# Optimization experiments

Hardware: AMD Instinct MI355X
Metric: run time of the kernel (lower is better)

## Reference

```python
import jax, jax.numpy as jnp
import numpy as np
from jax import lax

CONF_THRES = 0.25
IOU_THRES = 0.45
MAX_WH = 4096.0   # class offset, agnostic=False
MAX_DET = 300
NEG = jnp.float32(-1e30)


def setup_inputs() -> dict:
    key = jax.random.key(0)
    B, N, C = 16, 25200, 85  # 640x640 yolov5, nc=80
    k1, k2, k3, k4 = jax.random.split(key, 4)
    xy = jax.random.uniform(k1, (B, N, 2), jnp.float32, 0.0, 640.0)
    wh = jax.random.uniform(k2, (B, N, 2), jnp.float32, 4.0, 120.0)
    obj = jax.random.uniform(k3, (B, N, 1), jnp.float32)
    cls = jax.random.uniform(k4, (B, N, C - 5), jnp.float32)
    prediction = jnp.concatenate([xy, wh, obj, cls], axis=-1)
    return {"prediction": prediction}


def _xywh2xyxy(b):
    # b: [N,4] (cx,cy,w,h) -> (x1,y1,x2,y2)
    return jnp.concatenate([b[:, :2] - b[:, 2:4] * 0.5,
                            b[:, :2] + b[:, 2:4] * 0.5], axis=1)


def _iou_one_vs_all(box, boxes):
    # box: [4], boxes: [N,4], plain IoU as in torchvision.ops.nms
    x1 = jnp.maximum(box[0], boxes[:, 0])
    y1 = jnp.maximum(box[1], boxes[:, 1])
    x2 = jnp.minimum(box[2], boxes[:, 2])
    y2 = jnp.minimum(box[3], boxes[:, 3])
    inter = jnp.clip(x2 - x1, 0.0) * jnp.clip(y2 - y1, 0.0)
    a1 = (box[2] - box[0]) * (box[3] - box[1])
    a2 = (boxes[:, 2] - boxes[:, 0]) * (boxes[:, 3] - boxes[:, 1])
    return inter / (a1 + a2 - inter)


def _nms_image(p):
    # p: [N, 5+nc] single-image predictions (decoded xywh, obj, class scores)
    obj = p[:, 4]                               # [N]
    cls_scores = p[:, 5:] * obj[:, None]        # x[:,5:] *= x[:,4:5]
    conf = jnp.max(cls_scores, axis=1)          # best-class conf
    j = jnp.argmax(cls_scores, axis=1)          # best class id
    boxes = _xywh2xyxy(p[:, :4])                # [N,4]
    valid = (obj > CONF_THRES) & (conf > CONF_THRES)
    # class-offset boxes for per-class NMS (agnostic=False)
    nms_boxes = boxes + (j.astype(boxes.dtype) * MAX_WH)[:, None]

    s0 = jnp.where(valid, conf, NEG)

    def step(s_live, _):
        i = jnp.argmax(s_live)
        sel = s_live[i]
        keep = sel > 0.0
        iou = _iou_one_vs_all(nms_boxes[i], nms_boxes)
        suppress = keep & (iou > IOU_THRES)
        s_new = jnp.where(suppress, NEG, s_live).at[i].set(NEG)
        return s_new, (i, keep)

    _, (idxs, keeps) = lax.scan(step, s0, None, length=MAX_DET)
    # output rows [x1,y1,x2,y2,conf,cls] — boxes WITHOUT class offset
    rows = jnp.concatenate([boxes[idxs], conf[idxs, None],
                            j[idxs, None].astype(boxes.dtype)], axis=1)
    rows = rows * keeps[:, None].astype(rows.dtype)  # zero padded slots
    return rows, keeps


def reference(prediction):
    # prediction: [B, N, 5+nc] -> ([B, MAX_DET, 6], [B, MAX_DET] keep mask)
    out, keep = jax.vmap(_nms_image)(prediction)
    return out, keep
```

## Files before the change

### kernel.cpp

```cpp
#include <hip/hip_runtime.h>
#include <cstdint>
#include <cfloat>

#define BATCH 16
#define NBOX 25200
#define CH 85
#define NCLS 80
#define CAP 512
#define SEGCAP 128
#define ACC 32
#define MAXDET 300
#define RPB 112
#define CNTPAD 16

typedef unsigned long long u64;

__device__ __forceinline__ u64 shflx64(u64 v, int m) {
    int lo = __shfl_xor((int)(unsigned)(v & 0xffffffffu), m);
    int hi = __shfl_xor((int)(unsigned)(v >> 32), m);
    return ((u64)(unsigned)hi << 32) | (u64)(unsigned)lo;
}

__global__ __launch_bounds__(256) void pre_kernel(const float* __restrict__ p,
                                                  int* __restrict__ cnt,
                                                  u64* __restrict__ bucketKey,
                                                  float* __restrict__ outZero,
                                                  int outN) {
#pragma clang fp contract(off)
    __shared__ float s[RPB * CH];
    int tid = threadIdx.x;

    long z = (long)blockIdx.x * 256 + tid;
    if (z < outN) outZero[z] = 0.0f;

    long blockRow = (long)blockIdx.x * RPB;

    const float4* p4 = (const float4*)(p + blockRow * CH);
    float4* s4 = (float4*)s;
    for (int t = tid; t < RPB * CH / 4; t += 256) {
        __builtin_amdgcn_global_load_lds(
            (const __attribute__((address_space(1))) void*)(p4 + t),
            (__attribute__((address_space(3))) void*)(s4 + (t & ~63)),
            16, 0, 0);
    }
    __syncthreads();

    int r = tid >> 1;
    int half = tid & 1;
    if (r < RPB) {
        const float* row = s + r * CH;
        float obj = row[4];

        float v = -FLT_MAX; int c = 1000;
        int c0 = half * 40;
        for (int k = 0; k < 40; k++) {
            float sc = row[5 + c0 + k] * obj;
            int cc = c0 + k;
            if (sc > v) { v = sc; c = cc; }
        }
        float v2 = __shfl_xor(v, 1);
        int   cz = __shfl_xor(c, 1);
        if (v2 > v || (v2 == v && cz < c)) { v = v2; c = cz; }

        if (half == 0 && obj > 0.25f && v > 0.25f) {
            int wid = (int)blockRow + r;
            int b   = wid / NBOX;
            int idx = wid - b * NBOX;
            u64 key = ((u64)__float_as_uint(v) << 22) | ((u64)(32767 - idx) << 7) | (u64)c;
            int bkt = b * NCLS + c;
            int seg = idx & 3;
            int pos = atomicAdd(&cnt[bkt * CNTPAD + seg], 1);
            if (pos < SEGCAP) bucketKey[(long)bkt * CAP + seg * SEGCAP + pos] = key;
        }
    }
}

__global__ __launch_bounds__(64) void nms_kernel(const float* __restrict__ p,
                                                 const int* __restrict__ cnt,
                                                 const u64* __restrict__ bucketKey,
                                                 u64* __restrict__ accKey) {
#pragma clang fp contract(off)
    __shared__ float4 posBox[CAP];
    __shared__ u64    posKey[CAP];
    int lane = threadIdx.x;
    int bkt = blockIdx.x;
    int b = bkt / NCLS, c = bkt - b * NCLS;

    const int* cb = cnt + bkt * CNTPAD;
    int ns[4];
#pragma unroll
    for (int s2 = 0; s2 < 4; s2++) {
        int v = cb[s2];
        ns[s2] = (v < SEGCAP) ? v : SEGCAP;
    }

    u64 key[8];
#pragma unroll
    for (int r = 0; r < 8; r++) {
        u64 k = bucketKey[(long)bkt * CAP + (r << 6) + lane];
        int off = ((r & 1) << 6) | lane;
        key[r] = (off < ns[r >> 1]) ? k : 0ULL;
    }

#define CE_XL(K, LM)                                                    \
    { bool d = ((lane & ((K) >> 3)) == 0);                              \
      _Pragma("unroll")                                                 \
      for (int r = 0; r < 8; r++) {                                     \
          u64 part = shflx64(key[r], (LM));                             \
          bool up = ((lane & (LM)) == 0);                               \
          bool gt = key[r] > part;                                      \
          u64 mx = gt ? key[r] : part;                                  \
          u64 mn = gt ? part : key[r];                                  \
          key[r] = (d == up) ? mx : mn; } }
#define CE_RR(K, M)                                                    \
    { _Pragma("unroll")                                                \
      for (int r = 0; r < 8; r++) if (!(r & (M))) {                    \
          int r2 = r | (M);                                            \
          u64 a = key[r], e = key[r2];                                 \
          bool d = ((r & (K)) == 0);                                   \
          u64 hi = (a > e) ? a : e, lo = (a > e) ? e : a;              \
          key[r]  = d ? hi : lo;                                       \
          key[r2] = d ? lo : hi; } }
#define CE_RL(K, M)                                                    \
    { bool d = ((lane & ((K) >> 3)) == 0);                             \
      _Pragma("unroll")                                                \
      for (int r = 0; r < 8; r++) if (!(r & (M))) {                    \
          int r2 = r | (M);                                            \
          u64 a = key[r], e = key[r2];                                 \
          u64 hi = (a > e) ? a : e, lo = (a > e) ? e : a;              \
          key[r]  = d ? hi : lo;                                       \
          key[r2] = d ? lo : hi; } }

    CE_RR(2, 1)
    CE_RR(4, 2) CE_RR(4, 1)
    CE_RL(8, 4) CE_RL(8, 2) CE_RL(8, 1)
    CE_XL(16, 1)  CE_RL(16, 4)  CE_RL(16, 2)  CE_RL(16, 1)
    CE_XL(32, 2)  CE_XL(32, 1)  CE_RL(32, 4)  CE_RL(32, 2)  CE_RL(32, 1)
    CE_XL(64, 4)  CE_XL(64, 2)  CE_XL(64, 1)  CE_RL(64, 4)  CE_RL(64, 2)  CE_RL(64, 1)
    CE_XL(128, 8) CE_XL(128, 4) CE_XL(128, 2) CE_XL(128, 1)
    CE_RL(128, 4) CE_RL(128, 2) CE_RL(128, 1)
    CE_XL(256, 16) CE_XL(256, 8) CE_XL(256, 4) CE_XL(256, 2) CE_XL(256, 1)
    CE_RL(256, 4)  CE_RL(256, 2) CE_RL(256, 1)
    CE_XL(512, 32) CE_XL(512, 16) CE_XL(512, 8) CE_XL(512, 4) CE_XL(512, 2) CE_XL(512, 1)
    CE_RL(512, 4)  CE_RL(512, 2)  CE_RL(512, 1)
#undef CE_XL
#undef CE_RR
#undef CE_RL

    float x1[8], y1[8], x2[8], y2[8], ar[8];
    unsigned live = 0;
    float offc = (float)c * 4096.0f;
#pragma unroll
    for (int r = 0; r < 8; r++) {
        int t = (r << 6) | lane;
        posKey[t] = key[r];
        bool valid = key[r] != 0ULL;
        int idx = 32767 - (int)((key[r] >> 7) & 32767);
        const float* q = p + ((long)b * NBOX + (valid ? idx : 0)) * CH;
        float x = q[0], y = q[1], w = q[2], h = q[3];
        float hw = w * 0.5f, hh = h * 0.5f;
        x1[r] = (x - hw) + offc; y1[r] = (y - hh) + offc;
        x2[r] = (x + hw) + offc; y2[r] = (y + hh) + offc;
        ar[r] = (x2[r] - x1[r]) * (y2[r] - y1[r]);
        posBox[t] = make_float4(x1[r], y1[r], x2[r], y2[r]);
        if (valid) live |= 1u << r;
    }
    __syncthreads();

    long obase = (long)bkt * ACC;
    int nacc = 0;
    u64 mask = __ballot(live != 0);
    while (mask != 0ULL) {
        int L = (int)__ffsll((long long)mask) - 1;
        unsigned lv = (unsigned)__builtin_amdgcn_readlane((int)live, L);
        int r0 = __ffs((int)lv) - 1;
        int tp = (r0 << 6) | L;
        float4 B = posBox[tp];
        u64 kk = posKey[tp];
        if (lane == 0) accKey[obase + nacc] = kk;
        nacc++;
        if (lane == L) live &= ~(1u << r0);
        if (nacc == ACC) break;
        float A = (B.z - B.x) * (B.w - B.y);
#pragma unroll
        for (int r = 0; r < 8; r++) {
            if ((live >> r) & 1) {
                float xx1 = fmaxf(B.x, x1[r]);
                float yy1 = fmaxf(B.y, y1[r]);
                float xx2 = fminf(B.z, x2[r]);
                float yy2 = fminf(B.w, y2[r]);
                float inter = fmaxf(xx2 - xx1, 0.0f) * fmaxf(yy2 - yy1, 0.0f);
                float uni = (A + ar[r]) - inter;
                if (inter / uni > 0.45f) live &= ~(1u << r);
            }
        }
        mask = __ballot(live != 0);
    }
    for (int t2 = nacc + lane; t2 < ACC; t2 += 64) accKey[obase + t2] = 0ULL;
}

__global__ __launch_bounds__(256) void merge_kernel(const float* __restrict__ p,
                                                    const u64* __restrict__ accKey,
                                                    float* __restrict__ outRows,
                                                    float* __restrict__ outKeep) {
#pragma clang fp contract(off)
    __shared__ u64 L[NCLS * ACC];
    int tid = threadIdx.x;
    int b = blockIdx.y;
    const u64* src = accKey + (long)b * NCLS * ACC;
    for (int t = tid; t < NCLS * ACC; t += 256) L[t] = src[t];
    __syncthreads();

    int g = blockIdx.x * 256 + tid;
    u64 key = L[g];
    if (key == 0ULL) return;
    int cOwn = g / ACC;
    int rank = g - cOwn * ACC;

    int d = 1;
    for (; d + 3 < NCLS; d += 4) {
        int ca = cOwn + d;     if (ca >= NCLS) ca -= NCLS;
        int cb = cOwn + d + 1; if (cb >= NCLS) cb -= NCLS;
        int cc = cOwn + d + 2; if (cc >= NCLS) cc -= NCLS;
        int cd = cOwn + d + 3; if (cd >= NCLS) cd -= NCLS;
        const u64* LA = L + ca * ACC;
        const u64* LB = L + cb * ACC;
        const u64* LC = L + cc * ACC;
        const u64* LD = L + cd * ACC;
        int na = 0, nb = 0, nc = 0, nd = 0;
#pragma unroll
        for (int s2 = 32; s2; s2 >>= 1) {
            int ta = na + s2, tb = nb + s2, tc = nc + s2, td = nd + s2;
            if (ta <= ACC && LA[ta - 1] > key) na = ta;
            if (tb <= ACC && LB[tb - 1] > key) nb = tb;
            if (tc <= ACC && LC[tc - 1] > key) nc = tc;
            if (td <= ACC && LD[td - 1] > key) nd = td;
        }
        rank += na + nb + nc + nd;
        if (rank >= MAXDET) return;
    }
    for (; d < NCLS; d++) {
        int c2 = cOwn + d; if (c2 >= NCLS) c2 -= NCLS;
        const u64* Lc = L + c2 * ACC;
        int cn = 0;
#pragma unroll
        for (int s2 = 32; s2; s2 >>= 1) {
            int ncx = cn + s2;
            if (ncx <= ACC && Lc[ncx - 1] > key) cn = ncx;
        }
        rank += cn;
        if (rank >= MAXDET) return;
    }

    int cc  = (int)(key & 127);
    int idx = 32767 - (int)((key >> 7) & 32767);
    float conf = __uint_as_float((unsigned)(key >> 22));
    const float* q = p + ((long)b * NBOX + idx) * CH;
    float x = q[0], y = q[1], w = q[2], h = q[3];
    float hw = w * 0.5f, hh = h * 0.5f;
    float* row = outRows + ((long)b * MAXDET + rank) * 6;
    row[0] = x - hw; row[1] = y - hh; row[2] = x + hw; row[3] = y + hh;
    row[4] = conf;   row[5] = (float)cc;
    outKeep[b * MAXDET + rank] = 1.0f;
}

extern "C" void kernel_launch(void* const* d_in, const int* in_sizes, int n_in,
                              void* d_out, int out_size, void* d_ws, size_t ws_size,
                              hipStream_t stream) {
    const float* p = (const float*)d_in[0];
    float* out = (float*)d_out;

    char* ws = (char*)d_ws;
    int* cnt = (int*)ws;
    u64* bucketKey = (u64*)(ws + BATCH * NCLS * CNTPAD * 4);
    u64* accKey = (u64*)(ws + BATCH * NCLS * CNTPAD * 4
                            + (size_t)BATCH * NCLS * CAP * 8);

    hipMemsetAsync(cnt, 0, BATCH * NCLS * CNTPAD * sizeof(int), stream);
    pre_kernel<<<(BATCH * NBOX) / RPB, 256, 0, stream>>>(p, cnt, bucketKey, out, out_size);
    nms_kernel<<<BATCH * NCLS, 64, 0, stream>>>(p, cnt, bucketKey, accKey);
    dim3 gM(NCLS * ACC / 256, BATCH);
    merge_kernel<<<gM, 256, 0, stream>>>(p, accKey, out, out + (size_t)BATCH * MAXDET * 6);
}
```

Before: 278.8 us.

## Store precomputed boxes with keys in buckets and batch NMS picks eight at a time

Result: no change. 280.4 us (+0.6%).

```diff
diff --git a/kernel.cpp b/kernel.cpp
--- a/kernel.cpp
+++ b/kernel.cpp
@@ -23,7 +23,7 @@
 
 __global__ __launch_bounds__(256) void pre_kernel(const float* __restrict__ p,
                                                   int* __restrict__ cnt,
-                                                  u64* __restrict__ bucketKey,
+                                                  u64* __restrict__ rec,
                                                   float* __restrict__ outZero,
                                                   int outN) {
 #pragma clang fp contract(off)
@@ -70,21 +70,29 @@
             int bkt = b * NCLS + c;
             int seg = idx & 3;
             int pos = atomicAdd(&cnt[bkt * CNTPAD + seg], 1);
-            if (pos < SEGCAP) bucketKey[(long)bkt * CAP + seg * SEGCAP + pos] = key;
-        }
-    }
-}
-
-__global__ __launch_bounds__(64) void nms_kernel(const float* __restrict__ p,
-                                                 const int* __restrict__ cnt,
-                                                 const u64* __restrict__ bucketKey,
+            if (pos < SEGCAP) {
+                float x = row[0], y = row[1], w = row[2], h = row[3];
+                float hw = w * 0.5f, hh = h * 0.5f;
+                float offc = (float)c * 4096.0f;
+                float4 b4;
+                b4.x = (x - hw) + offc; b4.y = (y - hh) + offc;
+                b4.z = (x + hw) + offc; b4.w = (y + hh) + offc;
+                u64* slot = rec + ((long)bkt * CAP + seg * SEGCAP + pos) * 4;
+                *(float4*)slot = b4;
+                slot[2] = key;
+            }
+        }
+    }
+}
+
+__global__ __launch_bounds__(64) void nms_kernel(const int* __restrict__ cnt,
+                                                 const u64* __restrict__ rec,
                                                  u64* __restrict__ accKey) {
 #pragma clang fp contract(off)
     __shared__ float4 posBox[CAP];
     __shared__ u64    posKey[CAP];
     int lane = threadIdx.x;
     int bkt = blockIdx.x;
-    int b = bkt / NCLS, c = bkt - b * NCLS;
 
     const int* cb = cnt + bkt * CNTPAD;
     int ns[4];
@@ -94,13 +102,19 @@
         ns[s2] = (v < SEGCAP) ? v : SEGCAP;
     }
 
+    const u64* R = rec + (long)bkt * CAP * 4;
     u64 key[8];
 #pragma unroll
     for (int r = 0; r < 8; r++) {
-        u64 k = bucketKey[(long)bkt * CAP + (r << 6) + lane];
+        int slot = (r << 6) | lane;
+        float4 b4 = *(const float4*)(R + (long)slot * 4);
+        u64 k = R[(long)slot * 4 + 2];
+        posBox[slot] = b4;
+        posKey[slot] = k;
         int off = ((r & 1) << 6) | lane;
-        key[r] = (off < ns[r >> 1]) ? k : 0ULL;
-    }
+        key[r] = (off < ns[r >> 1]) ? ((k << 9) | (u64)slot) : 0ULL;
+    }
+    __syncthreads();
 
 #define CE_XL(K, LM)                                                    \
     { bool d = ((lane & ((K) >> 3)) == 0);                              \
@@ -149,52 +163,104 @@
 
     float x1[8], y1[8], x2[8], y2[8], ar[8];
     unsigned live = 0;
-    float offc = (float)c * 4096.0f;
 #pragma unroll
     for (int r = 0; r < 8; r++) {
-        int t = (r << 6) | lane;
-        posKey[t] = key[r];
-        bool valid = key[r] != 0ULL;
-        int idx = 32767 - (int)((key[r] >> 7) & 32767);
-        const float* q = p + ((long)b * NBOX + (valid ? idx : 0)) * CH;
-        float x = q[0], y = q[1], w = q[2], h = q[3];
-        float hw = w * 0.5f, hh = h * 0.5f;
-        x1[r] = (x - hw) + offc; y1[r] = (y - hh) + offc;
-        x2[r] = (x + hw) + offc; y2[r] = (y + hh) + offc;
-        ar[r] = (x2[r] - x1[r]) * (y2[r] - y1[r]);
-        posBox[t] = make_float4(x1[r], y1[r], x2[r], y2[r]);
-        if (valid) live |= 1u << r;
-    }
-    __syncthreads();
+        int slot = (int)(key[r] & 511u);
+        float4 B = posBox[slot];
+        x1[r] = B.x; y1[r] = B.y; x2[r] = B.z; y2[r] = B.w;
+        ar[r] = (B.z - B.x) * (B.w - B.y);
+        if (key[r] != 0ULL) live |= 1u << r;
+    }
 
     long obase = (long)bkt * ACC;
     int nacc = 0;
-    u64 mask = __ballot(live != 0);
-    while (mask != 0ULL) {
-        int L = (int)__ffsll((long long)mask) - 1;
-        unsigned lv = (unsigned)__builtin_amdgcn_readlane((int)live, L);
-        int r0 = __ffs((int)lv) - 1;
-        int tp = (r0 << 6) | L;
-        float4 B = posBox[tp];
-        u64 kk = posKey[tp];
-        if (lane == 0) accKey[obase + nacc] = kk;
-        nacc++;
-        if (lane == L) live &= ~(1u << r0);
-        if (nacc == ACC) break;
-        float A = (B.z - B.x) * (B.w - B.y);
-#pragma unroll
-        for (int r = 0; r < 8; r++) {
-            if ((live >> r) & 1) {
-                float xx1 = fmaxf(B.x, x1[r]);
-                float yy1 = fmaxf(B.y, y1[r]);
-                float xx2 = fminf(B.z, x2[r]);
-                float yy2 = fminf(B.w, y2[r]);
-                float inter = fmaxf(xx2 - xx1, 0.0f) * fmaxf(yy2 - yy1, 0.0f);
-                float uni = (A + ar[r]) - inter;
-                if (inter / uni > 0.45f) live &= ~(1u << r);
+    u64 lmask = __ballot(live != 0);
+    while (lmask != 0ULL && nacc < ACC) {
+        u64 bs01 = 0, bs23 = 0;
+        u64 bp01 = 0, bp23 = 0;
+        int bn = 0;
+        u64 wm = lmask;
+        while (bn < 8 && wm != 0ULL) {
+            int L = (int)__ffsll((long long)wm) - 1;
+            unsigned lv = (unsigned)__builtin_amdgcn_readlane((int)live, L);
+            while (lv && bn < 8) {
+                int r0 = __ffs((int)lv) - 1;
+                lv &= lv - 1;
+                int klo;
+                switch (r0) {
+                    case 0: klo = __builtin_amdgcn_readlane((int)(key[0] & 0xffffffffu), L); break;
+                    case 1: klo = __builtin_amdgcn_readlane((int)(key[1] & 0xffffffffu), L); break;
+                    case 2: klo = __builtin_amdgcn_readlane((int)(key[2] & 0xffffffffu), L); break;
+                    case 3: klo = __builtin_amdgcn_readlane((int)(key[3] & 0xffffffffu), L); break;
+                    case 4: klo = __builtin_amdgcn_readlane((int)(key[4] & 0xffffffffu), L); break;
+                    case 5: klo = __builtin_amdgcn_readlane((int)(key[5] & 0xffffffffu), L); break;
+                    case 6: klo = __builtin_amdgcn_readlane((int)(key[6] & 0xffffffffu), L); break;
+                    default:klo = __builtin_amdgcn_readlane((int)(key[7] & 0xffffffffu), L); break;
+                }
+                u64 slot = (u64)(klo & 511);
+                u64 posn = (u64)((L << 3) | r0);
+                if (bn < 4) { bs01 |= slot << (16 * bn);       bp01 |= posn << (16 * bn); }
+                else        { bs23 |= slot << (16 * (bn - 4)); bp23 |= posn << (16 * (bn - 4)); }
+                bn++;
             }
-        }
-        mask = __ballot(live != 0);
+            wm &= wm - 1;
+        }
+
+        int pi = lane >> 3, pj = lane & 7;
+        u64 wi = (pi < 4) ? bs01 : bs23;
+        u64 wj = (pj < 4) ? bs01 : bs23;
+        int spi = (int)((wi >> (16 * (pi & 3))) & 0xFFFFu);
+        int spj = (int)((wj >> (16 * (pj & 3))) & 0xFFFFu);
+        float4 Bi = posBox[spi & 511];
+        float4 Bj = posBox[spj & 511];
+        float pxx1 = fmaxf(Bi.x, Bj.x), pyy1 = fmaxf(Bi.y, Bj.y);
+        float pxx2 = fminf(Bi.z, Bj.z), pyy2 = fminf(Bi.w, Bj.w);
+        float pint = fmaxf(pxx2 - pxx1, 0.0f) * fmaxf(pyy2 - pyy1, 0.0f);
+        float Ai = (Bi.z - Bi.x) * (Bi.w - Bi.y);
+        float Aj = (Bj.z - Bj.x) * (Bj.w - Bj.y);
+        float puni = (Ai + Aj) - pint;
+        bool supp = (pi < pj) && (pint / puni > 0.45f);
+        u64 M = __ballot(supp);
+
+        u64 pickedSpread = 0; unsigned picked8 = 0; int cnt2 = 0;
+        int room = ACC - nacc;
+        for (int k = 0; k < 8; k++) {
+            if (k >= bn || cnt2 >= room) break;
+            bool dead = ((M >> k) & pickedSpread) != 0ULL;
+            if (!dead) { pickedSpread |= 1ULL << (8 * k); picked8 |= 1u << k; cnt2++; }
+        }
+
+        if (lane < 8 && ((picked8 >> lane) & 1u)) {
+            u64 w = (lane < 4) ? bs01 : bs23;
+            int sp = (int)((w >> (16 * (lane & 3))) & 0xFFFFu);
+            int rk = __popc(picked8 & ((1u << lane) - 1u));
+            accKey[obase + nacc + rk] = posKey[sp & 511];
+        }
+        nacc += cnt2;
+
+#pragma unroll
+        for (int k = 0; k < 8; k++) {
+            if ((picked8 >> k) & 1u) {
+                int pp = (int)(((k < 4 ? bp01 : bp23) >> (16 * (k & 3))) & 0xFFFFu);
+                if (lane == (pp >> 3)) live &= ~(1u << (pp & 7));
+                int sp = (int)(((k < 4 ? bs01 : bs23) >> (16 * (k & 3))) & 0xFFFFu);
+                float4 B = posBox[sp & 511];
+                float A = (B.z - B.x) * (B.w - B.y);
+#pragma unroll
+                for (int r = 0; r < 8; r++) {
+                    if ((live >> r) & 1u) {
+                        float xx1 = fmaxf(B.x, x1[r]);
+                        float yy1 = fmaxf(B.y, y1[r]);
+                        float xx2 = fminf(B.z, x2[r]);
+                        float yy2 = fminf(B.w, y2[r]);
+                        float inter = fmaxf(xx2 - xx1, 0.0f) * fmaxf(yy2 - yy1, 0.0f);
+                        float uni = (A + ar[r]) - inter;
+                        if (inter / uni > 0.45f) live &= ~(1u << r);
+                    }
+                }
+            }
+        }
+        lmask = __ballot(live != 0);
     }
     for (int t2 = nacc + lane; t2 < ACC; t2 += 64) accKey[obase + t2] = 0ULL;
 }
@@ -272,13 +338,13 @@
 
     char* ws = (char*)d_ws;
     int* cnt = (int*)ws;
-    u64* bucketKey = (u64*)(ws + BATCH * NCLS * CNTPAD * 4);
+    u64* rec = (u64*)(ws + BATCH * NCLS * CNTPAD * 4);
     u64* accKey = (u64*)(ws + BATCH * NCLS * CNTPAD * 4
-                            + (size_t)BATCH * NCLS * CAP * 8);
+                            + (size_t)BATCH * NCLS * CAP * 32);
 
     hipMemsetAsync(cnt, 0, BATCH * NCLS * CNTPAD * sizeof(int), stream);
-    pre_kernel<<<(BATCH * NBOX) / RPB, 256, 0, stream>>>(p, cnt, bucketKey, out, out_size);
-    nms_kernel<<<BATCH * NCLS, 64, 0, stream>>>(p, cnt, bucketKey, accKey);
+    pre_kernel<<<(BATCH * NBOX) / RPB, 256, 0, stream>>>(p, cnt, rec, out, out_size);
+    nms_kernel<<<BATCH * NCLS, 64, 0, stream>>>(cnt, rec, accKey);
     dim3 gM(NCLS * ACC / 256, BATCH);
     merge_kernel<<<gM, 256, 0, stream>>>(p, accKey, out, out + (size_t)BATCH * MAXDET * 6);
 }
```
